# Optimization experiments

Hardware: AMD Instinct MI355X
Metric: run time of the kernel (lower is better)

## Reference

```python
import jax, jax.numpy as jnp
import numpy as np

N_NODES = 100000
N_EDGES = 1600000
N_LABEL = 200000
IN_CH, HID_CH, OUT_CH = 64, 128, 64


def setup_inputs() -> dict:
    key = jax.random.key(0)
    ks = jax.random.split(key, 9)
    glorot = lambda k, fi, fo: jax.random.normal(k, (fi, fo), jnp.float32) * (2.0 / (fi + fo)) ** 0.5
    return {
        "x": jax.random.normal(ks[0], (N_NODES, IN_CH), jnp.float32),
        "W_l1": glorot(ks[1], IN_CH, HID_CH),
        "W_r1": glorot(ks[2], IN_CH, HID_CH),
        "b1": jnp.zeros((HID_CH,), jnp.float32),
        "W_l2": glorot(ks[3], HID_CH, OUT_CH),
        "W_r2": glorot(ks[4], HID_CH, OUT_CH),
        "b2": jnp.zeros((OUT_CH,), jnp.float32),
        "edge_index": jax.random.randint(ks[5], (2, N_EDGES), 0, N_NODES, jnp.int64 if jax.config.jax_enable_x64 else jnp.int32),
        "edge_label_index": jax.random.randint(ks[6], (2, N_LABEL), 0, N_NODES, jnp.int64 if jax.config.jax_enable_x64 else jnp.int32),
    }


def _sage_conv(x, edge_index, W_l, W_r, b):
    # PyG SAGEConv (mean aggr): out = lin_l(mean_{j in N(i)} x_j) + lin_r(x_i)
    src, dst = edge_index[0], edge_index[1]
    msg = x[src]                                             # [E, d] gather
    agg = jax.ops.segment_sum(msg, dst, num_segments=x.shape[0])  # [N, d]
    cnt = jax.ops.segment_sum(jnp.ones((edge_index.shape[1], 1), x.dtype), dst,
                              num_segments=x.shape[0])       # [N, 1]
    mean = agg / jnp.maximum(cnt, 1.0)                       # isolated nodes -> 0
    return mean @ W_l + x @ W_r + b


def reference(x, W_l1, W_r1, b1, W_l2, W_r2, b2, edge_index, edge_label_index):
    # encode (inference mode: dropout is identity)
    h = jax.nn.relu(_sage_conv(x, edge_index, W_l1, W_r1, b1))
    z = _sage_conv(h, edge_index, W_l2, W_r2, b2)            # [N, out]
    # decode: dot-product link scores
    src = z[edge_label_index[0]]                             # [P, out]
    dst = z[edge_label_index[1]]
    return jnp.sum(src * dst, axis=-1)                       # [P]
```

## Files before the change

### kernel.cpp

```cpp
#include <hip/hip_runtime.h>
#include <hip/hip_bf16.h>


#define NBUCK 512
#define NPB   200
#define WI    64

typedef __attribute__((ext_vector_type(4))) float f32x4;
typedef __attribute__((ext_vector_type(4))) int i32x4;
typedef __attribute__((ext_vector_type(2))) unsigned int u32x2;
typedef __attribute__((ext_vector_type(4))) unsigned short u16x4;
typedef __attribute__((ext_vector_type(8))) unsigned short u16x8;
typedef __attribute__((ext_vector_type(8))) short s16x8;

__device__ inline unsigned short f2bf(float f) {
    unsigned u = __float_as_uint(f);
    u += 0x7fffu + ((u >> 16) & 1u);
    return (unsigned short)(u >> 16);
}
__device__ inline float bf2f(unsigned short h) {
    return __uint_as_float(((unsigned)h) << 16);
}
__device__ inline unsigned int pk4_fp8(float a, float b, float c, float d) {
    int w = __builtin_amdgcn_cvt_pk_fp8_f32(a, b, 0, false);
    w = __builtin_amdgcn_cvt_pk_fp8_f32(c, d, w, true);
    return (unsigned int)w;
}
__device__ inline unsigned char one_fp8(float a) {
    return (unsigned char)(__builtin_amdgcn_cvt_pk_fp8_f32(a, a, 0, false) & 0xFF);
}

__global__ __launch_bounds__(256) void k_prep(const float* __restrict__ x,
                                              const float* __restrict__ Wl1,
                                              const float* __restrict__ Wr1,
                                              const float* __restrict__ Wl2,
                                              const float* __restrict__ Wr2,
                                              unsigned short* __restrict__ w1t,
                                              unsigned short* __restrict__ w2t,
                                              unsigned short* __restrict__ xb,
                                              unsigned int* __restrict__ xq,
                                              long long nx) {
    if (blockIdx.x < 16) {
        int id = (blockIdx.x * 256 + threadIdx.x) * 8;
        int which = id >> 14;
        int r0 = id & 16383;
#pragma unroll
        for (int i = 0; i < 8; ++i) {
            int r = r0 + i;
            int n = r >> 7, k = r & 127;
            float v;
            if (which == 0) v = (k < 64) ? Wl1[k * 128 + n] : Wr1[(k - 64) * 128 + n];
            else            v = (n < 64) ? Wl2[k * 64 + n] : Wr2[k * 64 + (n - 64)];
            (which ? w2t : w1t)[r] = f2bf(v);
        }
        return;
    }
    long long i = ((long long)(blockIdx.x - 16) * 256 + threadIdx.x) * 8;
    if (i + 8 > nx) return;
    f32x4 a = __builtin_nontemporal_load((const f32x4*)(x + i));
    f32x4 b = __builtin_nontemporal_load((const f32x4*)(x + i + 4));
    u16x8 o;
    o[0] = f2bf(a.x); o[1] = f2bf(a.y); o[2] = f2bf(a.z); o[3] = f2bf(a.w);
    o[4] = f2bf(b.x); o[5] = f2bf(b.y); o[6] = f2bf(b.z); o[7] = f2bf(b.w);
    __builtin_nontemporal_store(o, (u16x8*)(xb + i));
    u32x2 q;
    q.x = pk4_fp8(a.x, a.y, a.z, a.w);
    q.y = pk4_fp8(b.x, b.y, b.z, b.w);
    __builtin_nontemporal_store(q, (u32x2*)(xq + (i >> 2)));
}

__global__ __launch_bounds__(256) void k_bucket(const int* __restrict__ ei, int E,
                                                int capB,
                                                int* __restrict__ buckets,
                                                int* __restrict__ meta,
                                                int* __restrict__ ovfA) {
    __shared__ int lcnt[NBUCK];
    __shared__ int lbase[NBUCK];
    __shared__ int lidx[NBUCK];
    const int t = threadIdx.x;
    const int e0 = blockIdx.x * 4096;
    for (int i = t; i < NBUCK; i += 256) { lcnt[i] = 0; lidx[i] = 0; }
    __syncthreads();

    int s[16], d[16], b[16];
    bool v[16];
#pragma unroll
    for (int r = 0; r < 4; ++r) {
        int e = e0 + r * 1024 + t * 4;
        i32x4 s4, d4;
        if (e + 4 <= E) {
            s4 = __builtin_nontemporal_load((const i32x4*)(ei + e));
            d4 = __builtin_nontemporal_load((const i32x4*)(ei + E + e));
        } else {
            s4.x = (e < E) ? ei[e] : 0;         d4.x = (e < E) ? ei[E + e] : 0;
            s4.y = (e + 1 < E) ? ei[e + 1] : 0; d4.y = (e + 1 < E) ? ei[E + e + 1] : 0;
            s4.z = (e + 2 < E) ? ei[e + 2] : 0; d4.z = (e + 2 < E) ? ei[E + e + 2] : 0;
            s4.w = (e + 3 < E) ? ei[e + 3] : 0; d4.w = (e + 3 < E) ? ei[E + e + 3] : 0;
        }
        s[r * 4 + 0] = s4.x; s[r * 4 + 1] = s4.y; s[r * 4 + 2] = s4.z; s[r * 4 + 3] = s4.w;
        d[r * 4 + 0] = d4.x; d[r * 4 + 1] = d4.y; d[r * 4 + 2] = d4.z; d[r * 4 + 3] = d4.w;
        v[r * 4 + 0] = (e < E); v[r * 4 + 1] = (e + 1 < E);
        v[r * 4 + 2] = (e + 2 < E); v[r * 4 + 3] = (e + 3 < E);
    }
#pragma unroll
    for (int k = 0; k < 16; ++k) {
        b[k] = (unsigned)d[k] / NPB;
        if (v[k]) atomicAdd(&lcnt[b[k]], 1);
    }
    __syncthreads();
    for (int i = t; i < NBUCK; i += 256) {
        int c = lcnt[i];
        lbase[i] = (c > 0) ? atomicAdd(&meta[i], c) : 0;
    }
    __syncthreads();
#pragma unroll
    for (int k = 0; k < 16; ++k) {
        if (!v[k]) continue;
        int slot = atomicAdd(&lidx[b[k]], 1);
        int pos = lbase[b[k]] + slot;
        if (pos < capB) {
            int local = d[k] - b[k] * NPB;
            buckets[(size_t)b[k] * capB + pos] = (local << 17) | s[k];
        } else {
            int oi = atomicAdd(&meta[NBUCK], 1);
            ovfA[(size_t)oi * 2] = s[k];
            ovfA[(size_t)oi * 2 + 1] = d[k];
        }
    }
}

__global__ __launch_bounds__(256) void k_fill_lds(const int* __restrict__ buckets,
                                                  int capB,
                                                  const int* __restrict__ meta_ro,
                                                  int* __restrict__ deg,
                                                  int* __restrict__ ell, int N) {
    __shared__ int cur[NPB];
    __shared__ int ells[NPB * WI];
    const int t = threadIdx.x;
    const int b = blockIdx.x;
    const int base = b * NPB;
    for (int i = t; i < NPB; i += 256) cur[i] = 0;
    __syncthreads();
    const int cnt = min(meta_ro[b], capB);
    const int* bk = buckets + (size_t)b * capB;
    for (int i = t; i < cnt; i += 256) {
        unsigned v = (unsigned)__builtin_nontemporal_load(bk + i);
        int s = (int)(v & 0x1FFFFu);
        int local = (int)(v >> 17);
        int slot = atomicAdd(&cur[local], 1);
        if (slot < WI) ells[local * WI + slot] = s;
    }
    __syncthreads();
    const int nn = min(NPB, N - base);
    if (nn <= 0) return;
    for (int i = t; i < nn; i += 256) deg[base + i] = cur[i];
    const int lim = nn * WI;
    for (int j = t * 4; j < lim; j += 256 * 4) {
        if ((j & (WI - 1)) >= cur[j >> 6]) continue;
        i32x4 vv = *(const i32x4*)&ells[j];
        __builtin_nontemporal_store(vv, (i32x4*)(ell + (size_t)base * WI + j));
    }
}

__global__ __launch_bounds__(256) void k_fill_list(const int* __restrict__ ovfA,
                                                   const int* __restrict__ meta_ro,
                                                   int* __restrict__ deg,
                                                   int* __restrict__ ell) {
    const int cnt = meta_ro[NBUCK];
    for (int i = blockIdx.x * 256 + threadIdx.x; i < cnt; i += gridDim.x * 256) {
        int s = ovfA[(size_t)i * 2];
        int d = ovfA[(size_t)i * 2 + 1];
        int pos = atomicAdd(&deg[d], 1);
        if (pos < WI) ell[(size_t)d * WI + pos] = s;
    }
}

__global__ __launch_bounds__(256) void k_agg_q(const unsigned int* __restrict__ featq,
                                               const int* __restrict__ deg,
                                               const int* __restrict__ ell,
                                               unsigned short* __restrict__ outb,
                                               const float* __restrict__ addend,
                                               int n) {
    const int node = blockIdx.x * 16 + (threadIdx.x >> 4);
    const int l = threadIdx.x & 15;
    if (node >= n) return;
    const int dg = deg[node];
    const int cnt = min(dg, WI);
    const int* row = ell + (size_t)node * WI;
    float ax = 0.f, ay = 0.f, az = 0.f, aw = 0.f;
    int j = 0;
    for (; j + 4 <= cnt; j += 4) {
        i32x4 s4 = __builtin_nontemporal_load((const i32x4*)(row + j));
        int a = (int)featq[(size_t)s4.x * 16 + l];
        int b = (int)featq[(size_t)s4.y * 16 + l];
        int c = (int)featq[(size_t)s4.z * 16 + l];
        int d = (int)featq[(size_t)s4.w * 16 + l];
        ax += __builtin_amdgcn_cvt_f32_fp8(a, 0) + __builtin_amdgcn_cvt_f32_fp8(b, 0)
            + __builtin_amdgcn_cvt_f32_fp8(c, 0) + __builtin_amdgcn_cvt_f32_fp8(d, 0);
        ay += __builtin_amdgcn_cvt_f32_fp8(a, 1) + __builtin_amdgcn_cvt_f32_fp8(b, 1)
            + __builtin_amdgcn_cvt_f32_fp8(c, 1) + __builtin_amdgcn_cvt_f32_fp8(d, 1);
        az += __builtin_amdgcn_cvt_f32_fp8(a, 2) + __builtin_amdgcn_cvt_f32_fp8(b, 2)
            + __builtin_amdgcn_cvt_f32_fp8(c, 2) + __builtin_amdgcn_cvt_f32_fp8(d, 2);
        aw += __builtin_amdgcn_cvt_f32_fp8(a, 3) + __builtin_amdgcn_cvt_f32_fp8(b, 3)
            + __builtin_amdgcn_cvt_f32_fp8(c, 3) + __builtin_amdgcn_cvt_f32_fp8(d, 3);
    }
    for (; j < cnt; ++j) {
        int s = __builtin_nontemporal_load(row + j);
        int a = (int)featq[(size_t)s * 16 + l];
        ax += __builtin_amdgcn_cvt_f32_fp8(a, 0);
        ay += __builtin_amdgcn_cvt_f32_fp8(a, 1);
        az += __builtin_amdgcn_cvt_f32_fp8(a, 2);
        aw += __builtin_amdgcn_cvt_f32_fp8(a, 3);
    }
    const float inv = 1.0f / (float)max(dg, 1);
    float vx = ax * inv, vy = ay * inv, vz = az * inv, vw = aw * inv;
    if (addend) {
        const f32x4 ad = *(const f32x4*)(addend + (size_t)node * 64 + l * 4);
        vx += ad.x; vy += ad.y; vz += ad.z; vw += ad.w;
    }
    u16x4 ob;
    ob[0] = f2bf(vx); ob[1] = f2bf(vy); ob[2] = f2bf(vz); ob[3] = f2bf(vw);
    __builtin_nontemporal_store(ob, (u16x4*)(outb + (size_t)node * 64 + l * 4));
}

__global__ __launch_bounds__(256) void k_gemm1_mfma(
    const unsigned short* __restrict__ mean1b,
    const unsigned short* __restrict__ xb,
    const unsigned short* __restrict__ w1t,
    const float* __restrict__ b1,
    unsigned short* __restrict__ h, int M) {
    __shared__ unsigned short Wl[128 * 128];
    __shared__ unsigned short Cst[4][32 * 136];
    const int t = threadIdx.x;
    const int wv = t >> 6, l = t & 63;
    const int lr = l & 15, lq = l >> 4;
    const int row0 = blockIdx.x * 128 + wv * 32;

    const s16x8 zf = {0, 0, 0, 0, 0, 0, 0, 0};
    s16x8 af[2][4];
#pragma unroll
    for (int mt = 0; mt < 2; ++mt) {
        int r = row0 + mt * 16 + lr;
        bool ok = r < M;
#pragma unroll
        for (int ks = 0; ks < 4; ++ks) {
            int k = ks * 32 + lq * 8;
            const unsigned short* src = (k < 64) ? (mean1b + (size_t)r * 64 + k)
                                                 : (xb + (size_t)r * 64 + (k - 64));
            af[mt][ks] = ok ? *(const s16x8*)src : zf;
        }
    }
#pragma unroll
    for (int i = 0; i < 8; ++i) {
        int byte = (i * 256 + t) * 16;
        int swz = byte ^ (((byte >> 8) & 7) << 4);
        *(u16x8*)((char*)Wl + swz) = *(const u16x8*)((const char*)w1t + byte);
    }
    __syncthreads();
    if (row0 >= M) return;

    f32x4 acc[2][8];
#pragma unroll
    for (int mt = 0; mt < 2; ++mt)
#pragma unroll
        for (int nt = 0; nt < 8; ++nt) {
            f32x4 z = {0.f, 0.f, 0.f, 0.f};
            acc[mt][nt] = z;
        }
#pragma unroll
    for (int nt = 0; nt < 8; ++nt) {
        int n = nt * 16 + lr;
#pragma unroll
        for (int ks = 0; ks < 4; ++ks) {
            int byte = (n * 256 + ks * 64 + lq * 16) ^ ((n & 7) << 4);
            s16x8 bf = *(const s16x8*)((const char*)Wl + byte);
            acc[0][nt] = __builtin_amdgcn_mfma_f32_16x16x32_bf16(af[0][ks], bf, acc[0][nt], 0, 0, 0);
            acc[1][nt] = __builtin_amdgcn_mfma_f32_16x16x32_bf16(af[1][ks], bf, acc[1][nt], 0, 0, 0);
        }
    }
    unsigned short* cs = &Cst[wv][0];
#pragma unroll
    for (int nt = 0; nt < 8; ++nt) {
        float bb = b1[nt * 16 + lr];
#pragma unroll
        for (int mt = 0; mt < 2; ++mt)
#pragma unroll
            for (int j = 0; j < 4; ++j) {
                float v = fmaxf(acc[mt][nt][j] + bb, 0.f);
                cs[(mt * 16 + lq * 4 + j) * 136 + nt * 16 + lr] = f2bf(v);
            }
    }
#pragma unroll
    for (int p = 0; p < 8; ++p) {
        int r = p * 4 + lq;
        int gr = row0 + r;
        if (gr < M) {
            u16x8 v = *(const u16x8*)&cs[r * 136 + lr * 8];
            __builtin_nontemporal_store(v, (u16x8*)(h + (size_t)gr * 128 + lr * 8));
        }
    }
}

__global__ __launch_bounds__(256) void k_gemm2_mfma(
    const unsigned short* __restrict__ h,
    const unsigned short* __restrict__ w2t,
    const float* __restrict__ b2,
    unsigned int* __restrict__ pq,
    float* __restrict__ zb, int M) {
    __shared__ unsigned short Wl[128 * 128];
    __shared__ __align__(16) char Cst[4][8704];
    const int t = threadIdx.x;
    const int wv = t >> 6, l = t & 63;
    const int lr = l & 15, lq = l >> 4;
    const int row0 = blockIdx.x * 128 + wv * 32;

    const s16x8 zf = {0, 0, 0, 0, 0, 0, 0, 0};
    s16x8 af[2][4];
#pragma unroll
    for (int mt = 0; mt < 2; ++mt) {
        int r = row0 + mt * 16 + lr;
        bool ok = r < M;
#pragma unroll
        for (int ks = 0; ks < 4; ++ks)
            af[mt][ks] = ok ? *(const s16x8*)(h + (size_t)r * 128 + ks * 32 + lq * 8) : zf;
    }
#pragma unroll
    for (int i = 0; i < 8; ++i) {
        int byte = (i * 256 + t) * 16;
        int swz = byte ^ (((byte >> 8) & 7) << 4);
        *(u16x8*)((char*)Wl + swz) = *(const u16x8*)((const char*)w2t + byte);
    }
    __syncthreads();
    if (row0 >= M) return;

    f32x4 acc[2][8];
#pragma unroll
    for (int mt = 0; mt < 2; ++mt)
#pragma unroll
        for (int nt = 0; nt < 8; ++nt) {
            f32x4 z = {0.f, 0.f, 0.f, 0.f};
            acc[mt][nt] = z;
        }
#pragma unroll
    for (int nt = 0; nt < 8; ++nt) {
        int n = nt * 16 + lr;
#pragma unroll
        for (int ks = 0; ks < 4; ++ks) {
            int byte = (n * 256 + ks * 64 + lq * 16) ^ ((n & 7) << 4);
            s16x8 bf = *(const s16x8*)((const char*)Wl + byte);
            acc[0][nt] = __builtin_amdgcn_mfma_f32_16x16x32_bf16(af[0][ks], bf, acc[0][nt], 0, 0, 0);
            acc[1][nt] = __builtin_amdgcn_mfma_f32_16x16x32_bf16(af[1][ks], bf, acc[1][nt], 0, 0, 0);
        }
    }
    unsigned char* csb = (unsigned char*)&Cst[wv][0];
#pragma unroll
    for (int nt = 0; nt < 4; ++nt)
#pragma unroll
        for (int mt = 0; mt < 2; ++mt)
#pragma unroll
            for (int j = 0; j < 4; ++j)
                csb[(mt * 16 + lq * 4 + j) * 68 + nt * 16 + lr] = one_fp8(acc[mt][nt][j]);
#pragma unroll
    for (int p = 0; p < 8; ++p) {
        int r = p * 4 + lq;
        int gr = row0 + r;
        if (gr < M) {
            unsigned int v = *(const unsigned int*)&csb[r * 68 + lr * 4];
            __builtin_nontemporal_store(v, pq + (size_t)gr * 16 + lr);
        }
    }
    __syncthreads();
    float* csf = (float*)&Cst[wv][0];
#pragma unroll
    for (int nt = 4; nt < 8; ++nt) {
        int col = (nt - 4) * 16 + lr;
        float bb = b2[col];
#pragma unroll
        for (int mt = 0; mt < 2; ++mt)
#pragma unroll
            for (int j = 0; j < 4; ++j)
                csf[(mt * 16 + lq * 4 + j) * 68 + col] = acc[mt][nt][j] + bb;
    }
#pragma unroll
    for (int p = 0; p < 8; ++p) {
        int r = p * 4 + lq;
        int gr = row0 + r;
        if (gr < M) {
            f32x4 v = *(const f32x4*)&csf[r * 68 + lr * 4];
            __builtin_nontemporal_store(v, (f32x4*)(zb + (size_t)gr * 64 + lr * 4));
        }
    }
}

__global__ __launch_bounds__(256) void k_decode(const unsigned short* __restrict__ zq,
                                                const int* __restrict__ eli,
                                                float* __restrict__ out, int P) {
    int t = threadIdx.x;
    int g = blockIdx.x * 16 + (t >> 4);
    int l = t & 15;
    if (g >= P) return;
    int a = __builtin_nontemporal_load(eli + g);
    int b = __builtin_nontemporal_load(eli + P + g);
    u16x4 va = *(const u16x4*)(zq + (size_t)a * 64 + l * 4);
    u16x4 vb = *(const u16x4*)(zq + (size_t)b * 64 + l * 4);
    float s = bf2f(va[0]) * bf2f(vb[0]) + bf2f(va[1]) * bf2f(vb[1])
            + bf2f(va[2]) * bf2f(vb[2]) + bf2f(va[3]) * bf2f(vb[3]);
    s += __shfl_xor(s, 1);
    s += __shfl_xor(s, 2);
    s += __shfl_xor(s, 4);
    s += __shfl_xor(s, 8);
    if (l == 0) out[g] = s;
}

extern "C" void kernel_launch(void* const* d_in, const int* in_sizes, int n_in,
                              void* d_out, int out_size, void* d_ws, size_t ws_size,
                              hipStream_t stream) {
    const float* x   = (const float*)d_in[0];
    const float* Wl1 = (const float*)d_in[1];
    const float* Wr1 = (const float*)d_in[2];
    const float* b1  = (const float*)d_in[3];
    const float* Wl2 = (const float*)d_in[4];
    const float* Wr2 = (const float*)d_in[5];
    const float* b2  = (const float*)d_in[6];
    const int* ei  = (const int*)d_in[7];
    const int* eli = (const int*)d_in[8];
    const int N = in_sizes[0] / 64;
    const int E = in_sizes[7] / 2;
    const int P = in_sizes[8] / 2;
    float* out = (float*)d_out;

    const int capB = ((E / NBUCK) * 5 / 4 + 1024 + 3) & ~3;

    char* w = (char*)d_ws;
    auto alloc = [&](size_t bytes) {
        char* pp = w;
        w += (bytes + 255) & ~(size_t)255;
        return pp;
    };
    int* deg  = (int*)alloc((size_t)N * 4);
    int* meta = (int*)alloc(4096);
    int* ell  = (int*)alloc((size_t)N * WI * 4);
    unsigned short* xb     = (unsigned short*)alloc((size_t)N * 64 * 2);
    unsigned int*   xq     = (unsigned int*)alloc((size_t)N * 64);
    unsigned int*   pq     = (unsigned int*)alloc((size_t)N * 64);
    unsigned short* mean1b = (unsigned short*)alloc((size_t)N * 64 * 2);
    unsigned short* zq     = (unsigned short*)alloc((size_t)N * 64 * 2);
    unsigned short* w1t    = (unsigned short*)alloc(128 * 128 * 2);
    unsigned short* w2t    = (unsigned short*)alloc(128 * 128 * 2);
    size_t hb = (size_t)N * 128 * 2;
    size_t bb = (size_t)NBUCK * capB * 4 + 256 + (size_t)E * 8;
    char* hreg = alloc(hb > bb ? hb : bb);
    unsigned short* h = (unsigned short*)hreg;
    int* buckets = (int*)hreg;
    int* ovfA = (int*)(hreg + (((size_t)NBUCK * capB * 4 + 255) & ~(size_t)255));
    float* zb = (float*)alloc((size_t)N * 64 * 4);

    (void)hipMemsetAsync(meta, 0, 4096, stream);

    {
        long long n = (long long)N * 64;
        int xblocks = (int)((n / 8 + 255) / 256);
        k_prep<<<16 + xblocks, 256, 0, stream>>>(x, Wl1, Wr1, Wl2, Wr2,
                                                 w1t, w2t, xb, xq, n);
    }

    k_bucket<<<(E + 4095) / 4096, 256, 0, stream>>>(ei, E, capB, buckets, meta, ovfA);
    k_fill_lds<<<(N + NPB - 1) / NPB, 256, 0, stream>>>(buckets, capB, meta, deg, ell, N);
    k_fill_list<<<32, 256, 0, stream>>>(ovfA, meta, deg, ell);

    const int agg_grid = (N + 15) / 16;
    k_agg_q<<<agg_grid, 256, 0, stream>>>(xq, deg, ell, mean1b, nullptr, N);

    const int gemm_grid = (N + 127) / 128;
    k_gemm1_mfma<<<gemm_grid, 256, 0, stream>>>(mean1b, xb, w1t, b1, h, N);
    k_gemm2_mfma<<<gemm_grid, 256, 0, stream>>>(h, w2t, b2, pq, zb, N);

    k_agg_q<<<agg_grid, 256, 0, stream>>>(pq, deg, ell, zq, zb, N);

    k_decode<<<(P + 15) / 16, 256, 0, stream>>>(zq, eli, out, P);
}
```

Baseline: 171.9 us.

## Fuse both GEMMs via LDS, fold meta memset into prep, widen fp8 gather

The two MFMA GEMM kernels are merged into one, so the hidden activation h stays in LDS and is no longer written to and re-read from global memory. The meta memset is replaced by zeroing inside k_prep, which removes one stream operation. The aggregation loop is unrolled to 8 neighbors per step and uses packed fp8-to-f32 conversions where the builtin exists. The fused kernel needs roughly 100KB of LDS per block, which may lower occupancy.

```diff
diff --git a/kernel.cpp b/kernel.cpp
--- a/kernel.cpp
+++ b/kernel.cpp
@@ -6,6 +6,7 @@
 #define NPB   200
 #define WI    64
 
+typedef __attribute__((ext_vector_type(2))) float f32x2;
 typedef __attribute__((ext_vector_type(4))) float f32x4;
 typedef __attribute__((ext_vector_type(4))) int i32x4;
 typedef __attribute__((ext_vector_type(2))) unsigned int u32x2;
@@ -28,6 +29,17 @@
 }
 __device__ inline unsigned char one_fp8(float a) {
     return (unsigned char)(__builtin_amdgcn_cvt_pk_fp8_f32(a, a, 0, false) & 0xFF);
+}
+__device__ inline void acc_fp8(unsigned int a, f32x2& lo, f32x2& hi) {
+#if __has_builtin(__builtin_amdgcn_cvt_pk_f32_fp8)
+    lo += __builtin_amdgcn_cvt_pk_f32_fp8((int)a, false);
+    hi += __builtin_amdgcn_cvt_pk_f32_fp8((int)a, true);
+#else
+    lo.x += __builtin_amdgcn_cvt_f32_fp8((int)a, 0);
+    lo.y += __builtin_amdgcn_cvt_f32_fp8((int)a, 1);
+    hi.x += __builtin_amdgcn_cvt_f32_fp8((int)a, 2);
+    hi.y += __builtin_amdgcn_cvt_f32_fp8((int)a, 3);
+#endif
 }
 
 __global__ __launch_bounds__(256) void k_prep(const float* __restrict__ x,
@@ -39,8 +51,13 @@
                                               unsigned short* __restrict__ w2t,
                                               unsigned short* __restrict__ xb,
                                               unsigned int* __restrict__ xq,
+                                              int* __restrict__ meta,
                                               long long nx) {
     if (blockIdx.x < 16) {
+        if (blockIdx.x == 0) {
+            i32x4 z = {0, 0, 0, 0};
+            *(i32x4*)(meta + threadIdx.x * 4) = z;
+        }
         int id = (blockIdx.x * 256 + threadIdx.x) * 8;
         int which = id >> 14;
         int r0 = id & 16383;
@@ -187,33 +204,40 @@
     const int dg = deg[node];
     const int cnt = min(dg, WI);
     const int* row = ell + (size_t)node * WI;
-    float ax = 0.f, ay = 0.f, az = 0.f, aw = 0.f;
+    f32x2 lo = {0.f, 0.f}, hi = {0.f, 0.f};
     int j = 0;
-    for (; j + 4 <= cnt; j += 4) {
-        i32x4 s4 = __builtin_nontemporal_load((const i32x4*)(row + j));
-        int a = (int)featq[(size_t)s4.x * 16 + l];
-        int b = (int)featq[(size_t)s4.y * 16 + l];
-        int c = (int)featq[(size_t)s4.z * 16 + l];
-        int d = (int)featq[(size_t)s4.w * 16 + l];
-        ax += __builtin_amdgcn_cvt_f32_fp8(a, 0) + __builtin_amdgcn_cvt_f32_fp8(b, 0)
-            + __builtin_amdgcn_cvt_f32_fp8(c, 0) + __builtin_amdgcn_cvt_f32_fp8(d, 0);
-        ay += __builtin_amdgcn_cvt_f32_fp8(a, 1) + __builtin_amdgcn_cvt_f32_fp8(b, 1)
-            + __builtin_amdgcn_cvt_f32_fp8(c, 1) + __builtin_amdgcn_cvt_f32_fp8(d, 1);
-        az += __builtin_amdgcn_cvt_f32_fp8(a, 2) + __builtin_amdgcn_cvt_f32_fp8(b, 2)
-            + __builtin_amdgcn_cvt_f32_fp8(c, 2) + __builtin_amdgcn_cvt_f32_fp8(d, 2);
-        aw += __builtin_amdgcn_cvt_f32_fp8(a, 3) + __builtin_amdgcn_cvt_f32_fp8(b, 3)
-            + __builtin_amdgcn_cvt_f32_fp8(c, 3) + __builtin_amdgcn_cvt_f32_fp8(d, 3);
+    for (; j + 8 <= cnt; j += 8) {
+        i32x4 sA = __builtin_nontemporal_load((const i32x4*)(row + j));
+        i32x4 sB = __builtin_nontemporal_load((const i32x4*)(row + j + 4));
+        unsigned a0 = featq[(size_t)sA.x * 16 + l];
+        unsigned a1 = featq[(size_t)sA.y * 16 + l];
+        unsigned a2 = featq[(size_t)sA.z * 16 + l];
+        unsigned a3 = featq[(size_t)sA.w * 16 + l];
+        unsigned a4 = featq[(size_t)sB.x * 16 + l];
+        unsigned a5 = featq[(size_t)sB.y * 16 + l];
+        unsigned a6 = featq[(size_t)sB.z * 16 + l];
+        unsigned a7 = featq[(size_t)sB.w * 16 + l];
+        acc_fp8(a0, lo, hi); acc_fp8(a1, lo, hi);
+        acc_fp8(a2, lo, hi); acc_fp8(a3, lo, hi);
+        acc_fp8(a4, lo, hi); acc_fp8(a5, lo, hi);
+        acc_fp8(a6, lo, hi); acc_fp8(a7, lo, hi);
+    }
+    if (j + 4 <= cnt) {
+        i32x4 sA = __builtin_nontemporal_load((const i32x4*)(row + j));
+        unsigned a0 = featq[(size_t)sA.x * 16 + l];
+        unsigned a1 = featq[(size_t)sA.y * 16 + l];
+        unsigned a2 = featq[(size_t)sA.z * 16 + l];
+        unsigned a3 = featq[(size_t)sA.w * 16 + l];
+        acc_fp8(a0, lo, hi); acc_fp8(a1, lo, hi);
+        acc_fp8(a2, lo, hi); acc_fp8(a3, lo, hi);
+        j += 4;
     }
     for (; j < cnt; ++j) {
         int s = __builtin_nontemporal_load(row + j);
-        int a = (int)featq[(size_t)s * 16 + l];
-        ax += __builtin_amdgcn_cvt_f32_fp8(a, 0);
-        ay += __builtin_amdgcn_cvt_f32_fp8(a, 1);
-        az += __builtin_amdgcn_cvt_f32_fp8(a, 2);
-        aw += __builtin_amdgcn_cvt_f32_fp8(a, 3);
+        acc_fp8(featq[(size_t)s * 16 + l], lo, hi);
     }
     const float inv = 1.0f / (float)max(dg, 1);
-    float vx = ax * inv, vy = ay * inv, vz = az * inv, vw = aw * inv;
+    float vx = lo.x * inv, vy = lo.y * inv, vz = hi.x * inv, vw = hi.y * inv;
     if (addend) {
         const f32x4 ad = *(const f32x4*)(addend + (size_t)node * 64 + l * 4);
         vx += ad.x; vy += ad.y; vz += ad.z; vw += ad.w;
@@ -223,18 +247,23 @@
     __builtin_nontemporal_store(ob, (u16x4*)(outb + (size_t)node * 64 + l * 4));
 }
 
-__global__ __launch_bounds__(256) void k_gemm1_mfma(
+__global__ __launch_bounds__(256) void k_gemm_fused(
     const unsigned short* __restrict__ mean1b,
     const unsigned short* __restrict__ xb,
     const unsigned short* __restrict__ w1t,
+    const unsigned short* __restrict__ w2t,
     const float* __restrict__ b1,
-    unsigned short* __restrict__ h, int M) {
-    __shared__ unsigned short Wl[128 * 128];
-    __shared__ unsigned short Cst[4][32 * 136];
+    const float* __restrict__ b2,
+    unsigned int* __restrict__ pq,
+    float* __restrict__ zb, int M) {
+    __shared__ unsigned short W1s[128 * 128];
+    __shared__ unsigned short W2s[128 * 128];
+    __shared__ __align__(16) unsigned short HT[128 * 136];
     const int t = threadIdx.x;
     const int wv = t >> 6, l = t & 63;
     const int lr = l & 15, lq = l >> 4;
-    const int row0 = blockIdx.x * 128 + wv * 32;
+    const int wrow = wv * 32;
+    const int row0 = blockIdx.x * 128 + wrow;
 
     const s16x8 zf = {0, 0, 0, 0, 0, 0, 0, 0};
     s16x8 af[2][4];
@@ -254,7 +283,8 @@
     for (int i = 0; i < 8; ++i) {
         int byte = (i * 256 + t) * 16;
         int swz = byte ^ (((byte >> 8) & 7) << 4);
-        *(u16x8*)((char*)Wl + swz) = *(const u16x8*)((const char*)w1t + byte);
+        *(u16x8*)((char*)W1s + swz) = *(const u16x8*)((const char*)w1t + byte);
+        *(u16x8*)((char*)W2s + swz) = *(const u16x8*)((const char*)w2t + byte);
     }
     __syncthreads();
     if (row0 >= M) return;
@@ -273,12 +303,11 @@
 #pragma unroll
         for (int ks = 0; ks < 4; ++ks) {
             int byte = (n * 256 + ks * 64 + lq * 16) ^ ((n & 7) << 4);
-            s16x8 bf = *(const s16x8*)((const char*)Wl + byte);
+            s16x8 bf = *(const s16x8*)((const char*)W1s + byte);
             acc[0][nt] = __builtin_amdgcn_mfma_f32_16x16x32_bf16(af[0][ks], bf, acc[0][nt], 0, 0, 0);
             acc[1][nt] = __builtin_amdgcn_mfma_f32_16x16x32_bf16(af[1][ks], bf, acc[1][nt], 0, 0, 0);
         }
     }
-    unsigned short* cs = &Cst[wv][0];
 #pragma unroll
     for (int nt = 0; nt < 8; ++nt) {
         float bb = b1[nt * 16 + lr];
@@ -287,59 +316,23 @@
 #pragma unroll
             for (int j = 0; j < 4; ++j) {
                 float v = fmaxf(acc[mt][nt][j] + bb, 0.f);
-                cs[(mt * 16 + lq * 4 + j) * 136 + nt * 16 + lr] = f2bf(v);
+                HT[(wrow + mt * 16 + lq * 4 + j) * 136 + nt * 16 + lr] = f2bf(v);
             }
     }
-#pragma unroll
-    for (int p = 0; p < 8; ++p) {
-        int r = p * 4 + lq;
-        int gr = row0 + r;
-        if (gr < M) {
-            u16x8 v = *(const u16x8*)&cs[r * 136 + lr * 8];
-            __builtin_nontemporal_store(v, (u16x8*)(h + (size_t)gr * 128 + lr * 8));
-        }
-    }
-}
-
-__global__ __launch_bounds__(256) void k_gemm2_mfma(
-    const unsigned short* __restrict__ h,
-    const unsigned short* __restrict__ w2t,
-    const float* __restrict__ b2,
-    unsigned int* __restrict__ pq,
-    float* __restrict__ zb, int M) {
-    __shared__ unsigned short Wl[128 * 128];
-    __shared__ __align__(16) char Cst[4][8704];
-    const int t = threadIdx.x;
-    const int wv = t >> 6, l = t & 63;
-    const int lr = l & 15, lq = l >> 4;
-    const int row0 = blockIdx.x * 128 + wv * 32;
-
-    const s16x8 zf = {0, 0, 0, 0, 0, 0, 0, 0};
-    s16x8 af[2][4];
-#pragma unroll
-    for (int mt = 0; mt < 2; ++mt) {
-        int r = row0 + mt * 16 + lr;
-        bool ok = r < M;
+    s16x8 af2[2][4];
+#pragma unroll
+    for (int mt = 0; mt < 2; ++mt)
 #pragma unroll
         for (int ks = 0; ks < 4; ++ks)
-            af[mt][ks] = ok ? *(const s16x8*)(h + (size_t)r * 128 + ks * 32 + lq * 8) : zf;
-    }
-#pragma unroll
-    for (int i = 0; i < 8; ++i) {
-        int byte = (i * 256 + t) * 16;
-        int swz = byte ^ (((byte >> 8) & 7) << 4);
-        *(u16x8*)((char*)Wl + swz) = *(const u16x8*)((const char*)w2t + byte);
-    }
-    __syncthreads();
-    if (row0 >= M) return;
-
-    f32x4 acc[2][8];
+            af2[mt][ks] = *(const s16x8*)&HT[(wrow + mt * 16 + lr) * 136 + ks * 32 + lq * 8];
+
+    f32x4 acc2[2][8];
 #pragma unroll
     for (int mt = 0; mt < 2; ++mt)
 #pragma unroll
         for (int nt = 0; nt < 8; ++nt) {
             f32x4 z = {0.f, 0.f, 0.f, 0.f};
-            acc[mt][nt] = z;
+            acc2[mt][nt] = z;
         }
 #pragma unroll
     for (int nt = 0; nt < 8; ++nt) {
@@ -347,19 +340,20 @@
 #pragma unroll
         for (int ks = 0; ks < 4; ++ks) {
             int byte = (n * 256 + ks * 64 + lq * 16) ^ ((n & 7) << 4);
-            s16x8 bf = *(const s16x8*)((const char*)Wl + byte);
-            acc[0][nt] = __builtin_amdgcn_mfma_f32_16x16x32_bf16(af[0][ks], bf, acc[0][nt], 0, 0, 0);
-            acc[1][nt] = __builtin_amdgcn_mfma_f32_16x16x32_bf16(af[1][ks], bf, acc[1][nt], 0, 0, 0);
-        }
-    }
-    unsigned char* csb = (unsigned char*)&Cst[wv][0];
+            s16x8 bf = *(const s16x8*)((const char*)W2s + byte);
+            acc2[0][nt] = __builtin_amdgcn_mfma_f32_16x16x32_bf16(af2[0][ks], bf, acc2[0][nt], 0, 0, 0);
+            acc2[1][nt] = __builtin_amdgcn_mfma_f32_16x16x32_bf16(af2[1][ks], bf, acc2[1][nt], 0, 0, 0);
+        }
+    }
+    char* scratch = (char*)&HT[(size_t)wrow * 136];
+    unsigned char* csb = (unsigned char*)scratch;
 #pragma unroll
     for (int nt = 0; nt < 4; ++nt)
 #pragma unroll
         for (int mt = 0; mt < 2; ++mt)
 #pragma unroll
             for (int j = 0; j < 4; ++j)
-                csb[(mt * 16 + lq * 4 + j) * 68 + nt * 16 + lr] = one_fp8(acc[mt][nt][j]);
+                csb[(mt * 16 + lq * 4 + j) * 68 + nt * 16 + lr] = one_fp8(acc2[mt][nt][j]);
 #pragma unroll
     for (int p = 0; p < 8; ++p) {
         int r = p * 4 + lq;
@@ -370,7 +364,7 @@
         }
     }
     __syncthreads();
-    float* csf = (float*)&Cst[wv][0];
+    float* csf = (float*)scratch;
 #pragma unroll
     for (int nt = 4; nt < 8; ++nt) {
         int col = (nt - 4) * 16 + lr;
@@ -379,7 +373,7 @@
         for (int mt = 0; mt < 2; ++mt)
 #pragma unroll
             for (int j = 0; j < 4; ++j)
-                csf[(mt * 16 + lq * 4 + j) * 68 + col] = acc[mt][nt][j] + bb;
+                csf[(mt * 16 + lq * 4 + j) * 68 + col] = acc2[mt][nt][j] + bb;
     }
 #pragma unroll
     for (int p = 0; p < 8; ++p) {
@@ -447,21 +441,17 @@
     unsigned short* zq     = (unsigned short*)alloc((size_t)N * 64 * 2);
     unsigned short* w1t    = (unsigned short*)alloc(128 * 128 * 2);
     unsigned short* w2t    = (unsigned short*)alloc(128 * 128 * 2);
-    size_t hb = (size_t)N * 128 * 2;
     size_t bb = (size_t)NBUCK * capB * 4 + 256 + (size_t)E * 8;
-    char* hreg = alloc(hb > bb ? hb : bb);
-    unsigned short* h = (unsigned short*)hreg;
-    int* buckets = (int*)hreg;
-    int* ovfA = (int*)(hreg + (((size_t)NBUCK * capB * 4 + 255) & ~(size_t)255));
+    char* breg = alloc(bb);
+    int* buckets = (int*)breg;
+    int* ovfA = (int*)(breg + (((size_t)NBUCK * capB * 4 + 255) & ~(size_t)255));
     float* zb = (float*)alloc((size_t)N * 64 * 4);
-
-    (void)hipMemsetAsync(meta, 0, 4096, stream);
 
     {
         long long n = (long long)N * 64;
         int xblocks = (int)((n / 8 + 255) / 256);
         k_prep<<<16 + xblocks, 256, 0, stream>>>(x, Wl1, Wr1, Wl2, Wr2,
-                                                 w1t, w2t, xb, xq, n);
+                                                 w1t, w2t, xb, xq, meta, n);
     }
 
     k_bucket<<<(E + 4095) / 4096, 256, 0, stream>>>(ei, E, capB, buckets, meta, ovfA);
@@ -472,8 +462,7 @@
     k_agg_q<<<agg_grid, 256, 0, stream>>>(xq, deg, ell, mean1b, nullptr, N);
 
     const int gemm_grid = (N + 127) / 128;
-    k_gemm1_mfma<<<gemm_grid, 256, 0, stream>>>(mean1b, xb, w1t, b1, h, N);
-    k_gemm2_mfma<<<gemm_grid, 256, 0, stream>>>(h, w2t, b2, pq, zb, N);
+    k_gemm_fused<<<gemm_grid, 256, 0, stream>>>(mean1b, xb, w1t, w2t, b1, b2, pq, zb, N);
 
     k_agg_q<<<agg_grid, 256, 0, stream>>>(pq, deg, ell, zq, zb, N);
 
```

Result: faster. 155.9 us (-9.3%).
